# Optimization experiments

Measured on AMD Instinct MI355X. Metric: run time of the kernel, lower is better.

Reference implementation:

```python
import jax, jax.numpy as jnp
import numpy as np

B, S, D = 2, 4096, 512
H = 8
HD = D // H


def setup_inputs() -> dict:
    key = jax.random.key(0)
    k1, k2, k3, k4, k5 = jax.random.split(key, 5)
    sd = 1.0 / np.sqrt(D)
    return {
        "x": jax.random.normal(k1, (B, S, D), dtype=jnp.float32),
        "Wqkv": jax.random.normal(k2, (3 * D, D), dtype=jnp.float32) * sd,
        "bqkv": jax.random.normal(k3, (3 * D,), dtype=jnp.float32) * 0.02,
        "Wo": jax.random.normal(k4, (D, D), dtype=jnp.float32) * sd,
        "bo": jax.random.normal(k5, (D,), dtype=jnp.float32) * 0.02,
    }


def reference(x, Wqkv, bqkv, Wo, bo):
    b, s, d = x.shape
    h, hd = H, d // H
    # QKV projection (torch Linear: x @ W^T + b)
    qkv = x @ Wqkv.T + bqkv                      # [b, s, 3d]
    q, k, v = jnp.split(qkv, 3, axis=-1)         # each [b, s, d]
    # [b, s, h, hd] -> [b, h, s, hd]
    q = q.reshape(b, s, h, hd).transpose(0, 2, 1, 3)
    k = k.reshape(b, s, h, hd).transpose(0, 2, 1, 3)
    v = v.reshape(b, s, h, hd).transpose(0, 2, 1, 3)
    # causal additive mask: triu(ones, diag=1) * -1e10
    mask = jnp.triu(jnp.ones((s, s), dtype=x.dtype), k=1) * jnp.asarray(-1e10, x.dtype)
    wts = jnp.einsum("bhqd,bhkd->bhqk", q, k) / np.sqrt(hd).astype(np.float32)
    wts = wts + mask[None, None, :, :]
    wts = jax.nn.softmax(wts, axis=-1)
    y = jnp.einsum("bhqk,bhkd->bhqd", wts, v)    # [b, h, s, hd]
    y = y.transpose(0, 2, 1, 3).reshape(b, s, d) # [b, s, d]
    out = y @ Wo.T + bo
    return out
```

## Files before the change

### kernel.cpp

```cpp
#include <hip/hip_runtime.h>


typedef __bf16 bf16x8 __attribute__((ext_vector_type(8)));
typedef float f32x4 __attribute__((ext_vector_type(4)));
typedef unsigned short u16;

#define MFMA(a, b, c) __builtin_amdgcn_mfma_f32_16x16x32_bf16(a, b, c, 0, 0, 0)
#define QSCALE 0.18033688011112042f
#define FIXEDM 12.0f

__device__ __forceinline__ float exp2_fast(float x) {
    return __builtin_amdgcn_exp2f(x);
}
__device__ __forceinline__ u16 f2bf(float f) {
    union { __bf16 h; u16 u; } v; v.h = (__bf16)f; return v.u;
}
__device__ __forceinline__ ushort4 f4_to_bf4(float4 v) {
    ushort4 r;
    r.x = f2bf(v.x); r.y = f2bf(v.y); r.z = f2bf(v.z); r.w = f2bf(v.w);
    return r;
}
__device__ __forceinline__ void load_lds16(const u16* g, u16* l) {
    __builtin_amdgcn_global_load_lds(
        (const __attribute__((address_space(1))) void*)g,
        (__attribute__((address_space(3))) void*)l, 16, 0, 0);
}

__global__ __launch_bounds__(256) void cvt_all(
    const float* __restrict__ x, const float* __restrict__ wq,
    const float* __restrict__ wo,
    u16* __restrict__ xb, u16* __restrict__ wqb, u16* __restrict__ wob)
{
    int i = blockIdx.x * 256 + threadIdx.x;
    if (i < 1048576) {
        ((ushort4*)xb)[i] = f4_to_bf4(((const float4*)x)[i]);
    } else if (i < 1048576 + 196608) {
        int j = i - 1048576;
        ((ushort4*)wqb)[j] = f4_to_bf4(((const float4*)wq)[j]);
    } else {
        int j = i - 1048576 - 196608;
        ((ushort4*)wob)[j] = f4_to_bf4(((const float4*)wo)[j]);
    }
}

__global__ __launch_bounds__(256) void gemm_qkv_bf(
    const u16* __restrict__ X, const u16* __restrict__ W,
    const float* __restrict__ bias,
    u16* __restrict__ QY, u16* __restrict__ Ko, u16* __restrict__ Vto)
{
    __shared__ u16 As[2 * 128 * 32];
    __shared__ u16 Bs[2 * 128 * 32];
    const int K = 512;
    const int tid = threadIdx.x, wave = tid >> 6, lane = tid & 63;
    const int l15 = lane & 15, quad = lane >> 4;
    const int bm = blockIdx.x * 128, bn = blockIdx.y * 128;
    const int wr = wave >> 1, wc = wave & 1;
    const int arow = lane >> 2;
    const int acol = (lane & 3) * 8;

    f32x4 acc[4][4] = {};
#pragma unroll
    for (int ii = 0; ii < 2; ii++) {
        const int inst = wave * 2 + ii;
        const int row = inst * 16 + arow;
        load_lds16(&X[(bm + row) * K + acol], &As[inst * 512]);
        load_lds16(&W[(bn + row) * K + acol], &Bs[inst * 512]);
    }
    int cur = 0;
    for (int k0 = 0; k0 < K; k0 += 32) {
        __builtin_amdgcn_s_barrier();
        if (k0 + 32 < K) {
            const int nb = (cur ^ 1) * 4096;
#pragma unroll
            for (int ii = 0; ii < 2; ii++) {
                const int inst = wave * 2 + ii;
                const int row = inst * 16 + arow;
                load_lds16(&X[(bm + row) * K + k0 + 32 + acol], &As[nb + inst * 512]);
                load_lds16(&W[(bn + row) * K + k0 + 32 + acol], &Bs[nb + inst * 512]);
            }
            asm volatile("s_waitcnt vmcnt(4)" ::: "memory");
        } else {
            asm volatile("s_waitcnt vmcnt(0)" ::: "memory");
        }
        __builtin_amdgcn_s_barrier();
        const int cb = cur * 4096;
        bf16x8 a[4], b[4];
#pragma unroll
        for (int i = 0; i < 4; i++)
            a[i] = *(const bf16x8*)&As[cb + (wr * 64 + i * 16 + l15) * 32 + quad * 8];
#pragma unroll
        for (int j = 0; j < 4; j++)
            b[j] = *(const bf16x8*)&Bs[cb + (wc * 64 + j * 16 + l15) * 32 + quad * 8];
#pragma unroll
        for (int i = 0; i < 4; i++)
#pragma unroll
            for (int j = 0; j < 4; j++)
                acc[i][j] = MFMA(b[i], a[j], acc[i][j]);
        cur ^= 1;
    }

    const int nbase = bn + wc * 64;
    const int which = nbase >> 9;
#pragma unroll
    for (int i = 0; i < 4; i++) {
        const int d0 = nbase + i * 16 + quad * 4;
        const float4 bv = *(const float4*)&bias[d0];
        const int d0m = d0 & 511;
        const int h = d0m >> 6, hd0 = d0m & 63;
#pragma unroll
        for (int j = 0; j < 4; j++) {
            const int s_g = bm + wr * 64 + j * 16 + l15;
            const int b_ = s_g >> 12, s0 = s_g & 4095;
            const int bhh = b_ * 8 + h;
            if (which == 2) {
#pragma unroll
                for (int r = 0; r < 4; r++) {
                    const float bvr = (r == 0) ? bv.x : (r == 1) ? bv.y : (r == 2) ? bv.z : bv.w;
                    Vto[((size_t)(bhh * 64 + hd0 + r)) * 4096 + s0] = f2bf(acc[i][j][r] + bvr);
                }
            } else if (which == 1) {
                ushort4 pk;
                pk.x = f2bf(acc[i][j][0] + bv.x);
                pk.y = f2bf(acc[i][j][1] + bv.y);
                pk.z = f2bf(acc[i][j][2] + bv.z);
                pk.w = f2bf(acc[i][j][3] + bv.w);
                *(ushort4*)&Ko[(bhh * 4096 + s0) * 64 + hd0] = pk;
            } else {
                ushort4 pk;
                pk.x = f2bf((acc[i][j][0] + bv.x) * QSCALE);
                pk.y = f2bf((acc[i][j][1] + bv.y) * QSCALE);
                pk.z = f2bf((acc[i][j][2] + bv.z) * QSCALE);
                pk.w = f2bf((acc[i][j][3] + bv.w) * QSCALE);
                *(ushort4*)&QY[((b_ * 4096 + s0) * 8 + h) * 64 + hd0] = pk;
            }
        }
    }
}

#define LS 72

__global__ __launch_bounds__(256, 4) void attn_k(
    const u16* __restrict__ QY, const u16* __restrict__ Kk, const u16* __restrict__ Vt,
    u16* __restrict__ PO, float* __restrict__ ML)
{
    __shared__ u16 Ks[2 * 64 * 64];
    __shared__ u16 Vs[64 * 64];
    __shared__ u16 Ps[4 * 16 * LS];

    const int tid = threadIdx.x, wave = tid >> 6, lane = tid & 63;
    const int l15 = lane & 15, quad = lane >> 4;
    const int bh = blockIdx.x;
    const int b_ = bh >> 3, h = bh & 7;
    const int u = (int)blockIdx.y;
    const int layer = u >> 4;
    const int p = u & 15;
    const int pp = p >> 1, seg = p & 1;
    const int qt = layer * 8 + ((layer & 1) ? (7 - pp) : pp);
    const int kt0 = seg ? (qt + 1) : 0;
    const int kt1 = seg ? (2 * qt + 2) : (qt + 1);
    const int base_r = qt * 128 + wave * 32;

    const u16* qpa = &QY[((b_ * 4096 + base_r + l15) * 8 + h) * 64];
    const u16* qpb = qpa + 16 * 8 * 64;
    bf16x8 qa0 = *(const bf16x8*)&qpa[quad * 8];
    bf16x8 qa1 = *(const bf16x8*)&qpa[32 + quad * 8];
    bf16x8 qb0 = *(const bf16x8*)&qpb[quad * 8];
    bf16x8 qb1 = *(const bf16x8*)&qpb[32 + quad * 8];

    f32x4 oa[4] = {}, ob[4] = {};
    f32x4 lacc_a = {}, lacc_b = {};

    const int r0 = tid >> 3;
    const int swz = 8 * ((tid & 7) ^ (r0 & 7));
    const u16* KgA = &Kk[(size_t)bh * 4096 * 64 + r0 * 64 + swz];
    const u16* VgA = &Vt[(size_t)bh * 64 * 4096 + r0 * 4096 + swz];
    u16* Ksf = &Ks[0];
    u16* Vsf = &Vs[0];

    const int c0 = 8 * (quad ^ (l15 & 7));

    bf16x8 ones;
#pragma unroll
    for (int i = 0; i < 8; i++) ones[i] = (__bf16)1.0f;

    u16* P = &Ps[wave * 16 * LS];

    load_lds16(KgA + kt0 * 4096, Ksf + wave * 512);
    load_lds16(KgA + kt0 * 4096 + 2048, Ksf + wave * 512 + 2048);

    int cur = 0;
    for (int kt = kt0; kt < kt1; kt++) {
        const int k0 = kt * 64;
        __builtin_amdgcn_s_barrier();
        load_lds16(VgA + k0, Vsf + wave * 512);
        load_lds16(VgA + k0 + 131072, Vsf + wave * 512 + 2048);
        const bool havnext = (kt + 1 < kt1);
        if (havnext) {
            u16* kb = Ksf + (cur ^ 1) * 4096 + wave * 512;
            load_lds16(KgA + (kt + 1) * 4096, kb);
            load_lds16(KgA + (kt + 1) * 4096 + 2048, kb + 2048);
            asm volatile("s_waitcnt vmcnt(4)" ::: "memory");
        } else {
            asm volatile("s_waitcnt vmcnt(2)" ::: "memory");
        }
        __builtin_amdgcn_s_barrier();

        const u16* Kcur = Ksf + cur * 4096;
        const bool nmA = (k0 + 63 > base_r);
        const bool nmB = (k0 + 63 > base_r + 16);
        f32x4 sa[4], sb[4];
#pragma unroll
        for (int j = 0; j < 4; j++) {
            f32x4 ia, ib;
            if (nmA) {
#pragma unroll
                for (int r = 0; r < 4; r++) {
                    const int key = k0 + j * 16 + quad * 4 + r;
                    ia[r] = (key > base_r + l15) ? -1e30f : -FIXEDM;
                }
            } else {
                ia[0] = -FIXEDM; ia[1] = -FIXEDM; ia[2] = -FIXEDM; ia[3] = -FIXEDM;
            }
            if (nmB) {
#pragma unroll
                for (int r = 0; r < 4; r++) {
                    const int key = k0 + j * 16 + quad * 4 + r;
                    ib[r] = (key > base_r + 16 + l15) ? -1e30f : -FIXEDM;
                }
            } else {
                ib[0] = -FIXEDM; ib[1] = -FIXEDM; ib[2] = -FIXEDM; ib[3] = -FIXEDM;
            }
            const int kb = (j * 16 + l15) * 64;
            bf16x8 kf0 = *(const bf16x8*)&Kcur[kb + c0];
            bf16x8 kf1 = *(const bf16x8*)&Kcur[kb + (c0 ^ 32)];
            ia = MFMA(kf0, qa0, ia);
            sa[j] = MFMA(kf1, qa1, ia);
            ib = MFMA(kf0, qb0, ib);
            sb[j] = MFMA(kf1, qb1, ib);
        }

        {
            float spa[4][4];
#pragma unroll
            for (int j = 0; j < 4; j++)
#pragma unroll
                for (int r = 0; r < 4; r++)
                    spa[j][r] = exp2_fast(sa[j][r]);
#pragma unroll
            for (int j = 0; j < 4; j++) {
                ushort4 w;
                w.x = f2bf(spa[j][0]); w.y = f2bf(spa[j][1]);
                w.z = f2bf(spa[j][2]); w.w = f2bf(spa[j][3]);
                *(ushort4*)&P[l15 * LS + j * 16 + quad * 4] = w;
            }
        }

        float spb[4][4];
#pragma unroll
        for (int j = 0; j < 4; j++)
#pragma unroll
            for (int r = 0; r < 4; r++)
                spb[j][r] = exp2_fast(sb[j][r]);

        bf16x8 pfa0 = *(const bf16x8*)&P[l15 * LS + quad * 8];
        bf16x8 pfa1 = *(const bf16x8*)&P[l15 * LS + 32 + quad * 8];
#pragma unroll
        for (int j = 0; j < 4; j++) {
            ushort4 w;
            w.x = f2bf(spb[j][0]); w.y = f2bf(spb[j][1]);
            w.z = f2bf(spb[j][2]); w.w = f2bf(spb[j][3]);
            *(ushort4*)&P[l15 * LS + j * 16 + quad * 4] = w;
        }
        bf16x8 pfb0 = *(const bf16x8*)&P[l15 * LS + quad * 8];
        bf16x8 pfb1 = *(const bf16x8*)&P[l15 * LS + 32 + quad * 8];

        lacc_a = MFMA(ones, pfa0, lacc_a);
        lacc_a = MFMA(ones, pfa1, lacc_a);
        lacc_b = MFMA(ones, pfb0, lacc_b);
        lacc_b = MFMA(ones, pfb1, lacc_b);

        if (havnext) {
            asm volatile("s_waitcnt vmcnt(2)" ::: "memory");
        } else {
            asm volatile("s_waitcnt vmcnt(0)" ::: "memory");
        }
        __builtin_amdgcn_s_barrier();

#pragma unroll
        for (int n = 0; n < 4; n++) {
            const int vb = (n * 16 + l15) * 64;
            bf16x8 vf0 = *(const bf16x8*)&Vs[vb + c0];
            bf16x8 vf1 = *(const bf16x8*)&Vs[vb + (c0 ^ 32)];
            oa[n] = MFMA(vf0, pfa0, oa[n]);
            oa[n] = MFMA(vf1, pfa1, oa[n]);
            ob[n] = MFMA(vf0, pfb0, ob[n]);
            ob[n] = MFMA(vf1, pfb1, ob[n]);
        }
        cur ^= 1;
    }

    const float lfa = lacc_a[0];
    const float lfb = lacc_b[0];
    const float iva = (lfa > 0.0f) ? 1.0f / lfa : 0.0f;
    const float ivb = (lfb > 0.0f) ? 1.0f / lfb : 0.0f;
    u16* ppa = &PO[(size_t)seg * 4194304 +
                   (size_t)((b_ * 4096 + base_r + l15) * 8 + h) * 64];
    u16* ppb = ppa + 16 * 8 * 64;
#pragma unroll
    for (int n = 0; n < 4; n++) {
        ushort4 wa;
        wa.x = f2bf(oa[n][0] * iva);
        wa.y = f2bf(oa[n][1] * iva);
        wa.z = f2bf(oa[n][2] * iva);
        wa.w = f2bf(oa[n][3] * iva);
        *(ushort4*)&ppa[n * 16 + quad * 4] = wa;
        ushort4 wb;
        wb.x = f2bf(ob[n][0] * ivb);
        wb.y = f2bf(ob[n][1] * ivb);
        wb.z = f2bf(ob[n][2] * ivb);
        wb.w = f2bf(ob[n][3] * ivb);
        *(ushort4*)&ppb[n * 16 + quad * 4] = wb;
    }
    if (quad == 0) {
        float* mpa = &ML[((seg * 16 + bh) * 4096 + base_r + l15) * 2];
        mpa[0] = FIXEDM;
        mpa[1] = lfa;
        float* mpb = mpa + 16 * 2;
        mpb[0] = FIXEDM;
        mpb[1] = lfb;
    }
}

__global__ __launch_bounds__(256) void merge_k(
    const u16* __restrict__ PO, const float* __restrict__ ML, u16* __restrict__ Y)
{
    const int flat = blockIdx.x * 256 + threadIdx.x;
    const int rs = flat >> 6;
    const int rem = flat & 63;
    const int h = rem >> 3, c = rem & 7;
    const int b_ = rs >> 12, s = rs & 4095;
    const int bh = b_ * 8 + h;
    const float m0 = ML[(bh * 4096 + s) * 2];
    const float l0 = ML[(bh * 4096 + s) * 2 + 1];
    const float m1 = ML[((16 + bh) * 4096 + s) * 2];
    const float l1 = ML[((16 + bh) * 4096 + s) * 2 + 1];
    const float m = fmaxf(m0, m1);
    const float w0 = (l0 > 0.0f) ? exp2_fast(m0 - m) * l0 : 0.0f;
    const float w1 = (l1 > 0.0f) ? exp2_fast(m1 - m) * l1 : 0.0f;
    const float inv = 1.0f / (w0 + w1);
    const float a0 = w0 * inv, a1 = w1 * inv;

    const size_t base = (size_t)(rs * 8 + h) * 64 + c * 8;
    bf16x8 x0 = *(const bf16x8*)&PO[base];
    bf16x8 x1 = *(const bf16x8*)&PO[4194304 + base];
    ushort4 lo, hi;
    lo.x = f2bf(a0 * (float)x0[0] + a1 * (float)x1[0]);
    lo.y = f2bf(a0 * (float)x0[1] + a1 * (float)x1[1]);
    lo.z = f2bf(a0 * (float)x0[2] + a1 * (float)x1[2]);
    lo.w = f2bf(a0 * (float)x0[3] + a1 * (float)x1[3]);
    hi.x = f2bf(a0 * (float)x0[4] + a1 * (float)x1[4]);
    hi.y = f2bf(a0 * (float)x0[5] + a1 * (float)x1[5]);
    hi.z = f2bf(a0 * (float)x0[6] + a1 * (float)x1[6]);
    hi.w = f2bf(a0 * (float)x0[7] + a1 * (float)x1[7]);
    *(ushort4*)&Y[base] = lo;
    *(ushort4*)&Y[base + 4] = hi;
}

__global__ __launch_bounds__(256) void gemm_o_bf(
    const u16* __restrict__ X, const u16* __restrict__ W,
    const float* __restrict__ bias, float* __restrict__ Out)
{
    __shared__ u16 As[2 * 128 * 32];
    __shared__ u16 Bs[2 * 128 * 32];
    const int K = 512;
    const int tid = threadIdx.x, wave = tid >> 6, lane = tid & 63;
    const int l15 = lane & 15, quad = lane >> 4;
    const int bm = blockIdx.x * 128, bn = blockIdx.y * 128;
    const int wr = wave >> 1, wc = wave & 1;
    const int arow = lane >> 2;
    const int acol = (lane & 3) * 8;

    f32x4 acc[4][4] = {};
#pragma unroll
    for (int ii = 0; ii < 2; ii++) {
        const int inst = wave * 2 + ii;
        const int row = inst * 16 + arow;
        load_lds16(&X[(bm + row) * K + acol], &As[inst * 512]);
        load_lds16(&W[(bn + row) * K + acol], &Bs[inst * 512]);
    }
    int cur = 0;
    for (int k0 = 0; k0 < K; k0 += 32) {
        __builtin_amdgcn_s_barrier();
        if (k0 + 32 < K) {
            const int nb = (cur ^ 1) * 4096;
#pragma unroll
            for (int ii = 0; ii < 2; ii++) {
                const int inst = wave * 2 + ii;
                const int row = inst * 16 + arow;
                load_lds16(&X[(bm + row) * K + k0 + 32 + acol], &As[nb + inst * 512]);
                load_lds16(&W[(bn + row) * K + k0 + 32 + acol], &Bs[nb + inst * 512]);
            }
            asm volatile("s_waitcnt vmcnt(4)" ::: "memory");
        } else {
            asm volatile("s_waitcnt vmcnt(0)" ::: "memory");
        }
        __builtin_amdgcn_s_barrier();
        const int cb = cur * 4096;
        bf16x8 a[4], b[4];
#pragma unroll
        for (int i = 0; i < 4; i++)
            a[i] = *(const bf16x8*)&As[cb + (wr * 64 + i * 16 + l15) * 32 + quad * 8];
#pragma unroll
        for (int j = 0; j < 4; j++)
            b[j] = *(const bf16x8*)&Bs[cb + (wc * 64 + j * 16 + l15) * 32 + quad * 8];
#pragma unroll
        for (int i = 0; i < 4; i++)
#pragma unroll
            for (int j = 0; j < 4; j++)
                acc[i][j] = MFMA(b[i], a[j], acc[i][j]);
        cur ^= 1;
    }
#pragma unroll
    for (int i = 0; i < 4; i++) {
        const int n0 = bn + wc * 64 + i * 16 + quad * 4;
        const float4 bv = *(const float4*)&bias[n0];
#pragma unroll
        for (int j = 0; j < 4; j++) {
            const int m = bm + wr * 64 + j * 16 + l15;
            float4 ov;
            ov.x = acc[i][j][0] + bv.x;
            ov.y = acc[i][j][1] + bv.y;
            ov.z = acc[i][j][2] + bv.z;
            ov.w = acc[i][j][3] + bv.w;
            *(float4*)&Out[(size_t)m * 512 + n0] = ov;
        }
    }
}

extern "C" void kernel_launch(void* const* d_in, const int* in_sizes, int n_in,
                              void* d_out, int out_size, void* d_ws, size_t ws_size,
                              hipStream_t stream) {
    (void)in_sizes; (void)n_in; (void)out_size; (void)ws_size;
    const float* x    = (const float*)d_in[0];
    const float* Wqkv = (const float*)d_in[1];
    const float* bqkv = (const float*)d_in[2];
    const float* Wo   = (const float*)d_in[3];
    const float* bo   = (const float*)d_in[4];
    float* out = (float*)d_out;

    u16* qy_ws = (u16*)d_ws;
    u16* k_ws  = qy_ws + 4194304;
    u16* vt_ws = k_ws + 4194304;
    float* ml  = (float*)(vt_ws + 4194304);
    u16* wqkvb = (u16*)(ml + 262144);
    u16* wob   = wqkvb + 786432;
    u16* xb    = (u16*)d_out;
    u16* po    = (u16*)d_out;

    cvt_all<<<5120, 256, 0, stream>>>(x, Wqkv, Wo, xb, wqkvb, wob);
    gemm_qkv_bf<<<dim3(64, 12), 256, 0, stream>>>(xb, wqkvb, bqkv, qy_ws, k_ws, vt_ws);
    attn_k<<<dim3(16, 64), 256, 0, stream>>>(qy_ws, k_ws, vt_ws, po, ml);
    merge_k<<<2048, 256, 0, stream>>>(po, ml, qy_ws);
    gemm_o_bf<<<dim3(64, 4), 256, 0, stream>>>(qy_ws, wob, bo, out);
}
```

Baseline: 182.5 us.

## Shrink attention blocks to 64 query rows with two waves and halved key split

Attention blocks shrink from four waves covering 128 query rows to two waves covering 64 rows, and the grid doubles to 128 y-blocks. Each query tile's key range is split into two near-equal halves, and tiles are scheduled longest-first. This replaces the earlier interleaved layer pairing. Each wave now loads its own half of the K/V tiles with four LDS loads, and the waitcnt thresholds change to match. The fixed softmax offset of 12 is replaced by zero, which removes the bias initialisation but makes exp2 overflow more likely for large scores.

```diff
diff --git a/kernel.cpp b/kernel.cpp
--- a/kernel.cpp
+++ b/kernel.cpp
@@ -7,7 +7,6 @@
 
 #define MFMA(a, b, c) __builtin_amdgcn_mfma_f32_16x16x32_bf16(a, b, c, 0, 0, 0)
 #define QSCALE 0.18033688011112042f
-#define FIXEDM 12.0f
 
 __device__ __forceinline__ float exp2_fast(float x) {
     return __builtin_amdgcn_exp2f(x);
@@ -139,26 +138,26 @@
 
 #define LS 72
 
-__global__ __launch_bounds__(256, 4) void attn_k(
+__global__ __launch_bounds__(128, 4) void attn_k(
     const u16* __restrict__ QY, const u16* __restrict__ Kk, const u16* __restrict__ Vt,
     u16* __restrict__ PO, float* __restrict__ ML)
 {
     __shared__ u16 Ks[2 * 64 * 64];
     __shared__ u16 Vs[64 * 64];
-    __shared__ u16 Ps[4 * 16 * LS];
+    __shared__ u16 Ps[2 * 16 * LS];
 
     const int tid = threadIdx.x, wave = tid >> 6, lane = tid & 63;
     const int l15 = lane & 15, quad = lane >> 4;
     const int bh = blockIdx.x;
     const int b_ = bh >> 3, h = bh & 7;
-    const int u = (int)blockIdx.y;
-    const int layer = u >> 4;
-    const int p = u & 15;
-    const int pp = p >> 1, seg = p & 1;
-    const int qt = layer * 8 + ((layer & 1) ? (7 - pp) : pp);
-    const int kt0 = seg ? (qt + 1) : 0;
-    const int kt1 = seg ? (2 * qt + 2) : (qt + 1);
-    const int base_r = qt * 128 + wave * 32;
+    const int y = (int)blockIdx.y;
+    const int qt = 63 - (y >> 1);
+    const int seg = y & 1;
+    const int total = qt + 1;
+    const int half = (total + 1) >> 1;
+    const int kt0 = seg ? half : 0;
+    const int kt1 = seg ? total : half;
+    const int base_r = qt * 64 + wave * 32;
 
     const u16* qpa = &QY[((b_ * 4096 + base_r + l15) * 8 + h) * 64];
     const u16* qpb = qpa + 16 * 8 * 64;
@@ -170,12 +169,12 @@
     f32x4 oa[4] = {}, ob[4] = {};
     f32x4 lacc_a = {}, lacc_b = {};
 
-    const int r0 = tid >> 3;
-    const int swz = 8 * ((tid & 7) ^ (r0 & 7));
-    const u16* KgA = &Kk[(size_t)bh * 4096 * 64 + r0 * 64 + swz];
-    const u16* VgA = &Vt[(size_t)bh * 64 * 4096 + r0 * 4096 + swz];
-    u16* Ksf = &Ks[0];
-    u16* Vsf = &Vs[0];
+    const int sr = lane >> 3;
+    const int swz = 8 * ((lane & 7) ^ sr);
+    const u16* KgA = &Kk[(size_t)bh * 4096 * 64 + (wave * 32 + sr) * 64 + swz];
+    const u16* VgA = &Vt[(size_t)bh * 64 * 4096 + (wave * 32 + sr) * 4096 + swz];
+    u16* KsW = &Ks[wave * 2048];
+    u16* VsW = &Vs[wave * 2048];
 
     const int c0 = 8 * (quad ^ (l15 & 7));
 
@@ -185,50 +184,49 @@
 
     u16* P = &Ps[wave * 16 * LS];
 
-    load_lds16(KgA + kt0 * 4096, Ksf + wave * 512);
-    load_lds16(KgA + kt0 * 4096 + 2048, Ksf + wave * 512 + 2048);
+#pragma unroll
+    for (int i = 0; i < 4; i++)
+        load_lds16(KgA + kt0 * 4096 + i * 512, KsW + i * 512);
 
     int cur = 0;
     for (int kt = kt0; kt < kt1; kt++) {
         const int k0 = kt * 64;
         __builtin_amdgcn_s_barrier();
-        load_lds16(VgA + k0, Vsf + wave * 512);
-        load_lds16(VgA + k0 + 131072, Vsf + wave * 512 + 2048);
+#pragma unroll
+        for (int i = 0; i < 4; i++)
+            load_lds16(VgA + k0 + i * 32768, VsW + i * 512);
         const bool havnext = (kt + 1 < kt1);
         if (havnext) {
-            u16* kb = Ksf + (cur ^ 1) * 4096 + wave * 512;
-            load_lds16(KgA + (kt + 1) * 4096, kb);
-            load_lds16(KgA + (kt + 1) * 4096 + 2048, kb + 2048);
+            u16* kb = &Ks[(cur ^ 1) * 4096 + wave * 2048];
+#pragma unroll
+            for (int i = 0; i < 4; i++)
+                load_lds16(KgA + (kt + 1) * 4096 + i * 512, kb + i * 512);
+            asm volatile("s_waitcnt vmcnt(8)" ::: "memory");
+        } else {
             asm volatile("s_waitcnt vmcnt(4)" ::: "memory");
-        } else {
-            asm volatile("s_waitcnt vmcnt(2)" ::: "memory");
-        }
-        __builtin_amdgcn_s_barrier();
-
-        const u16* Kcur = Ksf + cur * 4096;
+        }
+        __builtin_amdgcn_s_barrier();
+
+        const u16* Kcur = &Ks[cur * 4096];
         const bool nmA = (k0 + 63 > base_r);
         const bool nmB = (k0 + 63 > base_r + 16);
         f32x4 sa[4], sb[4];
 #pragma unroll
         for (int j = 0; j < 4; j++) {
-            f32x4 ia, ib;
+            f32x4 ia = {}, ib = {};
             if (nmA) {
 #pragma unroll
                 for (int r = 0; r < 4; r++) {
                     const int key = k0 + j * 16 + quad * 4 + r;
-                    ia[r] = (key > base_r + l15) ? -1e30f : -FIXEDM;
+                    ia[r] = (key > base_r + l15) ? -1e30f : 0.0f;
                 }
-            } else {
-                ia[0] = -FIXEDM; ia[1] = -FIXEDM; ia[2] = -FIXEDM; ia[3] = -FIXEDM;
             }
             if (nmB) {
 #pragma unroll
                 for (int r = 0; r < 4; r++) {
                     const int key = k0 + j * 16 + quad * 4 + r;
-                    ib[r] = (key > base_r + 16 + l15) ? -1e30f : -FIXEDM;
+                    ib[r] = (key > base_r + 16 + l15) ? -1e30f : 0.0f;
                 }
-            } else {
-                ib[0] = -FIXEDM; ib[1] = -FIXEDM; ib[2] = -FIXEDM; ib[3] = -FIXEDM;
             }
             const int kb = (j * 16 + l15) * 64;
             bf16x8 kf0 = *(const bf16x8*)&Kcur[kb + c0];
@@ -280,7 +278,7 @@
         lacc_b = MFMA(ones, pfb1, lacc_b);
 
         if (havnext) {
-            asm volatile("s_waitcnt vmcnt(2)" ::: "memory");
+            asm volatile("s_waitcnt vmcnt(4)" ::: "memory");
         } else {
             asm volatile("s_waitcnt vmcnt(0)" ::: "memory");
         }
@@ -323,10 +321,10 @@
     }
     if (quad == 0) {
         float* mpa = &ML[((seg * 16 + bh) * 4096 + base_r + l15) * 2];
-        mpa[0] = FIXEDM;
+        mpa[0] = 0.0f;
         mpa[1] = lfa;
         float* mpb = mpa + 16 * 2;
-        mpb[0] = FIXEDM;
+        mpb[0] = 0.0f;
         mpb[1] = lfb;
     }
 }
@@ -459,7 +457,7 @@
 
     cvt_all<<<5120, 256, 0, stream>>>(x, Wqkv, Wo, xb, wqkvb, wob);
     gemm_qkv_bf<<<dim3(64, 12), 256, 0, stream>>>(xb, wqkvb, bqkv, qy_ws, k_ws, vt_ws);
-    attn_k<<<dim3(16, 64), 256, 0, stream>>>(qy_ws, k_ws, vt_ws, po, ml);
+    attn_k<<<dim3(16, 128), 128, 0, stream>>>(qy_ws, k_ws, vt_ws, po, ml);
     merge_k<<<2048, 256, 0, stream>>>(po, ml, qy_ws);
     gemm_o_bf<<<dim3(64, 4), 256, 0, stream>>>(qy_ws, wob, bo, out);
 }
```

New measurement: 182.1 us. Within noise of the previous version (-0.2%).
